# Performance work log

Measured on AMD Instinct MI355X. Metric: run time of the kernel, lower is better.

Reference implementation:

```python
import jax, jax.numpy as jnp
import numpy as np

S, N, V, E, H, L = 40, 256, 32000, 1024, 1024, 2


def _gru_step(x, h, wih, whh, bih, bhh):
    # PyTorch GRU cell, gate order [r, z, n]
    gi = x @ wih.T + bih          # (N, 3H)
    gh = h @ whh.T + bhh          # (N, 3H)
    ir, iz, inn = jnp.split(gi, 3, axis=-1)
    hr, hz, hn = jnp.split(gh, 3, axis=-1)
    r = jax.nn.sigmoid(ir + hr)
    z = jax.nn.sigmoid(iz + hz)
    n = jnp.tanh(inn + r * hn)
    return (1.0 - z) * n + z * h


def setup_inputs() -> dict:
    key = jax.random.key(0)
    ks = jax.random.split(key, 16)
    nrm = lambda k, shp: (jax.random.normal(k, shp, jnp.float32) * 0.05)
    return {
        "tokens": jax.random.randint(ks[0], (S, N), 0, V),
        "hidden": jnp.zeros((L, N, H), jnp.float32),
        "emb": nrm(ks[1], (V, E)),
        "enc_wih": nrm(ks[2], (L, 3 * H, E)),
        "enc_whh": nrm(ks[3], (L, 3 * H, H)),
        "enc_bih": nrm(ks[4], (L, 3 * H)),
        "enc_bhh": nrm(ks[5], (L, 3 * H)),
        "dec_wih": nrm(ks[6], (L, 3 * H, H)),
        "dec_whh": nrm(ks[7], (L, 3 * H, H)),
        "dec_bih": nrm(ks[8], (L, 3 * H)),
        "dec_bhh": nrm(ks[9], (L, 3 * H)),
        "attn_w": nrm(ks[10], (S, E + L * H)),
        "attn_b": nrm(ks[11], (S,)),
        "comb_w": nrm(ks[12], (H, 2 * H)),
        "comb_b": nrm(ks[13], (H,)),
    }


def reference(tokens, hidden, emb, enc_wih, enc_whh, enc_bih, enc_bhh,
              dec_wih, dec_whh, dec_bih, dec_bhh,
              attn_w, attn_b, comb_w, comb_b):
    x = emb[tokens]                      # (S, N, E) embedded input

    # ---- encoder: 2-layer GRU over the full sequence ----
    seq = x
    h_finals = []
    for l in range(L):
        wih, whh, bih, bhh = enc_wih[l], enc_whh[l], enc_bih[l], enc_bhh[l]
        def step(h, xt, wih=wih, whh=whh, bih=bih, bhh=bhh):
            h2 = _gru_step(xt, h, wih, whh, bih, bhh)
            return h2, h2
        hT, seq = jax.lax.scan(step, hidden[l], seq)
        h_finals.append(hT)
    h_n = jnp.stack(h_finals)            # (L, N, H)
    enc_out = jnp.swapaxes(seq, 0, 1)    # (N, S, H)

    # ---- attention decoder: scan over timesteps, carry decoder hidden ----
    def dec_step(h, emb_t):
        # h: (L, N, H), emb_t: (N, E)
        h_flat = jnp.swapaxes(h, 0, 1).reshape(N, L * H)
        logits = jnp.concatenate([emb_t, h_flat], axis=-1) @ attn_w.T + attn_b
        aw = jax.nn.softmax(logits, axis=-1)                   # (N, S)
        applied = jnp.einsum('ns,nsh->nh', aw, enc_out)        # (N, H)
        xcur = jax.nn.relu(
            jnp.concatenate([emb_t, applied], axis=-1) @ comb_w.T + comb_b)
        hs = []
        for l in range(L):
            hl = _gru_step(xcur, h[l], dec_wih[l], dec_whh[l],
                           dec_bih[l], dec_bhh[l])
            hs.append(hl)
            xcur = hl
        return jnp.stack(hs), xcur

    hT, outs = jax.lax.scan(dec_step, h_n, x)   # outs: (S, N, H)
    return outs, hT
```

## Files before the change

### kernel.cpp

```cpp
#include <hip/hip_runtime.h>
#include <hip/hip_bf16.h>

#define S_LEN 40
#define NB    256
#define EDIM  1024
#define HDIM  1024
#define NBLK  256
#define NTHR  768

typedef _Float16 f16;
typedef __attribute__((ext_vector_type(8))) _Float16 f16x8;
typedef __attribute__((ext_vector_type(4))) _Float16 f16x4;
typedef __attribute__((ext_vector_type(4))) float f32x4;

__device__ __forceinline__ float sigm(float x) {
    x = fminf(fmaxf(x, -30.f), 30.f);
    return 1.f / (1.f + __expf(-x));
}
__device__ __forceinline__ float tanh_fast(float x) {
    x = fminf(fmaxf(x, -15.f), 15.f);
    float e = __expf(2.f * x);
    return (e - 1.f) / (e + 1.f);
}

__device__ __forceinline__ void sysst_f16(f16* p, f16 v) {
    union { f16 f; unsigned short s; } u; u.f = v;
    unsigned int b = u.s;
    asm volatile("global_store_short %0, %1, off sc0 sc1" :: "v"(p), "v"(b) : "memory");
}

__device__ __forceinline__ void gbar1(unsigned* cnt, unsigned* gen) {
    asm volatile("s_waitcnt vmcnt(0)" ::: "memory");
    __syncthreads();
    if (threadIdx.x == 0) {
        unsigned g = __hip_atomic_load(gen, __ATOMIC_RELAXED, __HIP_MEMORY_SCOPE_AGENT);
        unsigned a = __hip_atomic_fetch_add(cnt, 1u, __ATOMIC_RELEASE, __HIP_MEMORY_SCOPE_AGENT);
        if (a == NBLK - 1) {
            __hip_atomic_store(cnt, 0u, __ATOMIC_RELAXED, __HIP_MEMORY_SCOPE_AGENT);
            __hip_atomic_fetch_add(gen, 1u, __ATOMIC_RELEASE, __HIP_MEMORY_SCOPE_AGENT);
        } else {
            while (__hip_atomic_load(gen, __ATOMIC_RELAXED, __HIP_MEMORY_SCOPE_AGENT) == g)
                __builtin_amdgcn_s_sleep(1);
        }
    }
    __syncthreads();
}

__device__ __forceinline__ void g2bar(unsigned* sync, unsigned xcd,
                                      unsigned M, unsigned NX) {
    asm volatile("s_waitcnt vmcnt(0)" ::: "memory");
    __syncthreads();
    if (threadIdx.x == 0) {
        unsigned* ggen = sync;
        unsigned* gcnt = sync + 1;
        unsigned* xa = sync + 16 + xcd * 16;
        unsigned g = __hip_atomic_load(ggen, __ATOMIC_RELAXED, __HIP_MEMORY_SCOPE_AGENT);
        unsigned a = __hip_atomic_fetch_add(xa, 1u, __ATOMIC_RELEASE, __HIP_MEMORY_SCOPE_AGENT);
        if (a == M - 1) {
            __hip_atomic_store(xa, 0u, __ATOMIC_RELAXED, __HIP_MEMORY_SCOPE_AGENT);
            unsigned b = __hip_atomic_fetch_add(gcnt, 1u, __ATOMIC_RELEASE, __HIP_MEMORY_SCOPE_AGENT);
            if (b == NX - 1) {
                __hip_atomic_store(gcnt, 0u, __ATOMIC_RELAXED, __HIP_MEMORY_SCOPE_AGENT);
                __hip_atomic_fetch_add(ggen, 1u, __ATOMIC_RELEASE, __HIP_MEMORY_SCOPE_AGENT);
            } else {
                while (__hip_atomic_load(ggen, __ATOMIC_RELAXED, __HIP_MEMORY_SCOPE_AGENT) == g)
                    __builtin_amdgcn_s_sleep(1);
            }
        } else {
            while (__hip_atomic_load(ggen, __ATOMIC_RELAXED, __HIP_MEMORY_SCOPE_AGENT) == g)
                __builtin_amdgcn_s_sleep(1);
        }
    }
    __syncthreads();
}

__global__ void k_init_sync(unsigned* s) {
    for (int k = threadIdx.x; k < 1024; k += 256) s[k] = 0;
}

__device__ __forceinline__ void probe_mn(int lane, int* mrow, int* ncol) {
    f16x8 pa, pb;
#pragma unroll
    for (int e = 0; e < 8; e++) {
        pa[e] = (f16)(float)(lane & 15);
        pb[e] = (f16)0.03125f;
    }
    f32x4 pacc = {0, 0, 0, 0};
    pacc = __builtin_amdgcn_mfma_f32_16x16x32_f16(pa, pb, pacc, 0, 0, 0);
#pragma unroll
    for (int r = 0; r < 4; r++) {
        int m = (int)(pacc[r] + 0.5f);
        int cg = ((lane >> 4) << 2) + r;
        mrow[r] = m;
        ncol[r] = (m == cg) ? (lane & 15) : cg;
    }
}

__global__ __launch_bounds__(256) void k_cvt4(const float* __restrict__ src,
                                              f16* __restrict__ dst, int n4) {
    int i = blockIdx.x * 256 + threadIdx.x;
    if (i < n4) {
        f32x4 v = ((const f32x4*)src)[i];
        f16x4 o = {(f16)v.x, (f16)v.y, (f16)v.z, (f16)v.w};
        ((f16x4*)dst)[i] = o;
    }
}
__global__ __launch_bounds__(256) void k_embed_cvt(const int* __restrict__ tok,
                                                   const float* __restrict__ emb,
                                                   f16* __restrict__ xe) {
    int b = blockIdx.x;
    int t = threadIdx.x;
    int token = tok[b];
    f32x4 v = ((const f32x4*)(emb + (size_t)token * EDIM))[t];
    f16x4 o = {(f16)v.x, (f16)v.y, (f16)v.z, (f16)v.w};
    ((f16x4*)(xe + (size_t)b * EDIM))[t] = o;
}

__device__ void gru_phase(
    char* lds, int cb, int rb, int tid, const int* mr, const int* nc,
    const f16* __restrict__ xsrc, const f16* __restrict__ hsrc,
    const f16* __restrict__ wih, const f16* __restrict__ whh,
    const float* __restrict__ bih, const float* __restrict__ bhh,
    f16* ho16, float* of_step, float* of_fin) {

    {
        constexpr int TOT = 8192;
        constexpr int IT = (TOT + NTHR - 1) / NTHR;
        f16x8 val[IT];
#pragma unroll
        for (int i = 0; i < IT; i++) {
            int c = tid + i * NTHR;
            if (c < TOT) {
                int isH = c >> 12;
                int cl = c & 4095;
                int row = cl >> 7, cc = cl & 127;
                const f16* src = (isH ? hsrc : xsrc) +
                                 (size_t)(rb + row) * 1024 + cc * 8;
                val[i] = *(const f16x8*)src;
            }
        }
#pragma unroll
        for (int i = 0; i < IT; i++) {
            int c = tid + i * NTHR;
            if (c < TOT) {
                int isH = c >> 12;
                int cl = c & 4095;
                int row = cl >> 7, cc = cl & 127;
                *(f16x8*)(lds + isH * 65536 + row * 2048 +
                          ((cc ^ (row & 7)) << 4)) = val[i];
            }
        }
    }
    __syncthreads();

    const int w = tid >> 6, lane = tid & 63;
    const int pair = w >> 1, kh = w & 1;
    const int gate = (pair >= 3) ? pair - 3 : pair;
    const int r0 = lane & 15, kk0 = (lane >> 4) * 8;
    const f16* B = ((pair < 3) ? wih : whh) + ((size_t)gate * HDIM + cb) * 1024;
    const f16* B0 = B + (size_t)r0 * 1024 + kk0 + kh * 512;
    const f16* B1 = B + (size_t)(r0 + 16) * 1024 + kk0 + kh * 512;
    const int abase = (pair < 3) ? 0 : 65536;
    const int swz = r0 & 7;
    const char* a0p = lds + abase + r0 * 2048;
    const char* a1p = lds + abase + (r0 + 16) * 2048;

    f32x4 acc00 = {0,0,0,0}, acc01 = {0,0,0,0}, acc10 = {0,0,0,0}, acc11 = {0,0,0,0};
#pragma unroll 4
    for (int k = 0; k < 512; k += 32) {
        int g = (kh * 512 + kk0 + k) >> 3;
        int off = (g ^ swz) << 4;
        f16x8 a0 = *(const f16x8*)(a0p + off);
        f16x8 a1 = *(const f16x8*)(a1p + off);
        f16x8 b0 = *(const f16x8*)(B0 + k);
        f16x8 b1 = *(const f16x8*)(B1 + k);
        acc00 = __builtin_amdgcn_mfma_f32_16x16x32_f16(a0, b0, acc00, 0, 0, 0);
        acc01 = __builtin_amdgcn_mfma_f32_16x16x32_f16(a0, b1, acc01, 0, 0, 0);
        acc10 = __builtin_amdgcn_mfma_f32_16x16x32_f16(a1, b0, acc10, 0, 0, 0);
        acc11 = __builtin_amdgcn_mfma_f32_16x16x32_f16(a1, b1, acc11, 0, 0, 0);
    }
    __syncthreads();

    float* red = (float*)lds;
    float* rw = red + w * 1024;
#pragma unroll
    for (int r = 0; r < 4; r++) {
        rw[mr[r] * 32 + nc[r]]             = acc00[r];
        rw[mr[r] * 32 + nc[r] + 16]        = acc01[r];
        rw[(mr[r] + 16) * 32 + nc[r]]      = acc10[r];
        rw[(mr[r] + 16) * 32 + nc[r] + 16] = acc11[r];
    }
    __syncthreads();

#pragma unroll
    for (int it = 0; it < 2; it++) {
        int i = tid + it * NTHR;
        if (i < 1024) {
            int rr = i >> 5, ccn = i & 31;
            int col = cb + ccn;
            int row = rb + rr;
            float gir = red[i]         + red[1024 + i];
            float giz = red[2048 + i]  + red[3072 + i];
            float gin = red[4096 + i]  + red[5120 + i];
            float ghr = red[6144 + i]  + red[7168 + i];
            float ghz = red[8192 + i]  + red[9216 + i];
            float ghn = red[10240 + i] + red[11264 + i];
            float r = sigm(gir + bih[col] + ghr + bhh[col]);
            float z = sigm(giz + bih[HDIM + col] + ghz + bhh[HDIM + col]);
            float n = tanh_fast(gin + bih[2 * HDIM + col] +
                                r * (ghn + bhh[2 * HDIM + col]));
            int gidx = col >> 3, within = col & 7;
            float hp = (float)*(const f16*)(lds + 65536 + rr * 2048 +
                                            ((gidx ^ (rr & 7)) << 4) + within * 2);
            float hn2 = (1.f - z) * n + z * hp;
            size_t idx = (size_t)row * HDIM + col;
            sysst_f16(ho16 + idx, (f16)hn2);
            if (of_step) of_step[idx] = hn2;
            if (of_fin)  of_fin[idx] = hn2;
        }
    }
}

__device__ void attn_phase(
    char* lds, int bid, int tid,
    const f16* __restrict__ xe_t, const f16* __restrict__ h0,
    const f16* __restrict__ h1,
    const f16* __restrict__ attn_w, const float* __restrict__ attn_b,
    const f16* __restrict__ enc16, f16* __restrict__ appl) {
    float* logit = (float*)(lds + 131072);
    float* awls  = logit + 64;
    const int n = bid;
    const int w = tid >> 6, lane = tid & 63;
    const size_t nrow = (size_t)n * 1024;

    {
        constexpr int TOT = 5504;
        constexpr int IT = (TOT + NTHR - 1) / NTHR;
        f16x8 val[IT];
#pragma unroll
        for (int i = 0; i < IT; i++) {
            int c = tid + i * NTHR;
            if (c < TOT) {
                if (c < 5120) {
                    int s = c >> 7, cc = c & 127;
                    val[i] = __builtin_nontemporal_load(
                        (const f16x8*)(enc16 + ((size_t)s * NB + n) * 1024 + cc * 8));
                } else {
                    int r = c - 5120;
                    const f16* src = (r < 128) ? (xe_t + nrow + r * 8)
                                   : (r < 256) ? (h0 + nrow + (r - 128) * 8)
                                               : (h1 + nrow + (r - 256) * 8);
                    val[i] = *(const f16x8*)src;
                }
            }
        }
#pragma unroll
        for (int i = 0; i < IT; i++) {
            int c = tid + i * NTHR;
            if (c < TOT) {
                if (c < 5120) *(f16x8*)(lds + c * 16) = val[i];
                else          *(f16x8*)(lds + 81920 + (c - 5120) * 16) = val[i];
            }
        }
    }
    __syncthreads();

    if (w < 10) {
#pragma unroll
        for (int si = 0; si < 4; si++) {
            int s = w * 4 + si;
            const f16* wrow = attn_w + (size_t)s * 3072;
            float acc = 0.f;
#pragma unroll
            for (int jj = 0; jj < 6; jj++) {
                int j = lane + jj * 64;
                f16x8 a = *(const f16x8*)(lds + 81920 + j * 16);
                f16x8 b = __builtin_nontemporal_load((const f16x8*)(wrow + j * 8));
#pragma unroll
                for (int e = 0; e < 8; e++)
                    acc = fmaf((float)a[e], (float)b[e], acc);
            }
            for (int o = 32; o; o >>= 1) acc += __shfl_down(acc, o);
            if (lane == 0) logit[s] = acc + attn_b[s];
        }
    }
    __syncthreads();

    if (w == 0) {
        float v = (lane < S_LEN) ? logit[lane] : -1e30f;
        float m = v;
        for (int o = 32; o; o >>= 1) m = fmaxf(m, __shfl_xor(m, o));
        float e = (lane < S_LEN) ? __expf(v - m) : 0.f;
        float sum = e;
        for (int o = 32; o; o >>= 1) sum += __shfl_xor(sum, o);
        if (lane < S_LEN) awls[lane] = e / sum;
    }
    __syncthreads();

    for (int col = tid; col < 1024; col += NTHR) {
        float acc = 0.f;
#pragma unroll
        for (int s = 0; s < S_LEN; s++)
            acc = fmaf(awls[s], (float)*(const f16*)(lds + s * 2048 + col * 2), acc);
        sysst_f16(appl + nrow + col, (f16)acc);
    }
}

__device__ void comb_phase(
    char* lds, int cb, int rb, int tid, const int* mr, const int* nc,
    const f16* __restrict__ xe_t, const f16* __restrict__ appl,
    const f16* __restrict__ Bw, const float* __restrict__ bias,
    f16* __restrict__ Cout) {

    {
        constexpr int TOT = 8192;
        constexpr int IT = (TOT + NTHR - 1) / NTHR;
        f16x8 val[IT];
#pragma unroll
        for (int i = 0; i < IT; i++) {
            int c = tid + i * NTHR;
            if (c < TOT) {
                int row = c >> 8, cc = c & 255;
                const f16* src = (cc < 128)
                    ? (xe_t + (size_t)(rb + row) * 1024 + cc * 8)
                    : (appl + (size_t)(rb + row) * 1024 + (cc - 128) * 8);
                val[i] = *(const f16x8*)src;
            }
        }
#pragma unroll
        for (int i = 0; i < IT; i++) {
            int c = tid + i * NTHR;
            if (c < TOT) {
                int row = c >> 8, cc = c & 255;
                *(f16x8*)(lds + row * 4096 + ((cc ^ (row & 7)) << 4)) = val[i];
            }
        }
    }
    __syncthreads();

    const int w = tid >> 6, lane = tid & 63;
    const int r0 = lane & 15, kk0 = (lane >> 4) * 8;
    const int c0 = (w * 64) / 12, c1 = ((w + 1) * 64) / 12;
    const f16* B0 = Bw + (size_t)(cb + r0) * 2048 + kk0;
    const f16* B1 = Bw + (size_t)(cb + r0 + 16) * 2048 + kk0;
    const int swz = r0 & 7;
    const char* a0p = lds + r0 * 4096;
    const char* a1p = lds + (r0 + 16) * 4096;

    f32x4 acc00 = {0,0,0,0}, acc01 = {0,0,0,0}, acc10 = {0,0,0,0}, acc11 = {0,0,0,0};
    for (int c = c0; c < c1; c++) {
        int g = (c * 32 + kk0) >> 3;
        int off = (g ^ swz) << 4;
        f16x8 a0 = *(const f16x8*)(a0p + off);
        f16x8 a1 = *(const f16x8*)(a1p + off);
        f16x8 b0 = *(const f16x8*)(B0 + c * 32);
        f16x8 b1 = *(const f16x8*)(B1 + c * 32);
        acc00 = __builtin_amdgcn_mfma_f32_16x16x32_f16(a0, b0, acc00, 0, 0, 0);
        acc01 = __builtin_amdgcn_mfma_f32_16x16x32_f16(a0, b1, acc01, 0, 0, 0);
        acc10 = __builtin_amdgcn_mfma_f32_16x16x32_f16(a1, b0, acc10, 0, 0, 0);
        acc11 = __builtin_amdgcn_mfma_f32_16x16x32_f16(a1, b1, acc11, 0, 0, 0);
    }
    __syncthreads();

    float* red = (float*)lds;
    float* rw = red + w * 1024;
#pragma unroll
    for (int r = 0; r < 4; r++) {
        rw[mr[r] * 32 + nc[r]]             = acc00[r];
        rw[mr[r] * 32 + nc[r] + 16]        = acc01[r];
        rw[(mr[r] + 16) * 32 + nc[r]]      = acc10[r];
        rw[(mr[r] + 16) * 32 + nc[r] + 16] = acc11[r];
    }
    __syncthreads();

#pragma unroll
    for (int it = 0; it < 2; it++) {
        int i = tid + it * NTHR;
        if (i < 1024) {
            float s = 0.f;
#pragma unroll
            for (int p = 0; p < 12; p++) s += red[p * 1024 + i];
            int rr = i >> 5, ccn = i & 31;
            s += bias[cb + ccn];
            s = fmaxf(s, 0.f);
            sysst_f16(Cout + (size_t)(rb + rr) * 1024 + cb + ccn, (f16)s);
        }
    }
}

__global__ __launch_bounds__(NTHR, 3) void k_mega(
    const f16* __restrict__ xe,
    f16* H0, f16* H1,
    const f16* __restrict__ w_eih, const f16* __restrict__ w_ehh,
    const float* __restrict__ enc_bih, const float* __restrict__ enc_bhh,
    const f16* __restrict__ w_dih, const f16* __restrict__ w_dhh,
    const float* __restrict__ dec_bih, const float* __restrict__ dec_bhh,
    const f16* __restrict__ w_attn, const float* __restrict__ attn_b,
    const f16* __restrict__ w_comb, const float* __restrict__ comb_b,
    f16* XC, f16* AP,
    float* out, unsigned* sync) {
    __shared__ char smem[131584];
    __shared__ unsigned s_meta[8];
    char* lds = smem;
    const int bid = blockIdx.x;
    const int tid = threadIdx.x;
    const int lane = tid & 63;
    const size_t NH = (size_t)NB * HDIM;

    int mr[4], nc[4];
    probe_mn(lane, mr, nc);

    if (tid == 0) {
        unsigned x;
        asm volatile("s_getreg_b32 %0, hwreg(20, 0, 32)" : "=s"(x));
        x &= 7;
        unsigned r = __hip_atomic_fetch_add(sync + 256 + x, 1u,
                                            __ATOMIC_RELAXED, __HIP_MEMORY_SCOPE_AGENT);
        s_meta[0] = x; s_meta[1] = r;
    }
    __syncthreads();
    gbar1(sync + 512, sync + 513);
    if (tid == 0) {
        unsigned M = __hip_atomic_load(sync + 256 + s_meta[0],
                                       __ATOMIC_RELAXED, __HIP_MEMORY_SCOPE_AGENT);
        unsigned nx = 0;
        bool uniform = true;
        for (int i = 0; i < 8; i++) {
            unsigned ci = __hip_atomic_load(sync + 256 + i, __ATOMIC_RELAXED,
                                            __HIP_MEMORY_SCOPE_AGENT);
            nx += (ci > 0) ? 1u : 0u;
            if (ci != 32) uniform = false;
        }
        s_meta[2] = M; s_meta[3] = nx;
        if (uniform) {
            s_meta[4] = (s_meta[0] * 4 + (s_meta[1] & 3)) * 32;
            s_meta[5] = (s_meta[1] >> 2) * 32;
        } else {
            s_meta[4] = (((unsigned)bid & 7) * 4 + (((unsigned)bid >> 3) & 3)) * 32;
            s_meta[5] = ((unsigned)bid >> 5) * 32;
        }
    }
    __syncthreads();
    const unsigned xcd = s_meta[0], M = s_meta[2], NX = s_meta[3];
    const int cb = (int)s_meta[4], rb = (int)s_meta[5];

    for (int t = 0; t < S_LEN; t++) {
        gru_phase(lds, cb, rb, tid, mr, nc,
                  xe + (size_t)t * NB * EDIM, H0 + (size_t)t * NH,
                  w_eih, w_ehh, enc_bih, enc_bhh,
                  H0 + (size_t)(t + 1) * NH, (float*)nullptr, (float*)nullptr);
        g2bar(sync, xcd, M, NX);
    }
    for (int t = 0; t < S_LEN; t++) {
        gru_phase(lds, cb, rb, tid, mr, nc,
                  H0 + (size_t)(t + 1) * NH, H1 + (size_t)t * NH,
                  w_eih + (size_t)3 * HDIM * EDIM, w_ehh + (size_t)3 * HDIM * HDIM,
                  enc_bih + 3 * HDIM, enc_bhh + 3 * HDIM,
                  H1 + (size_t)(t + 1) * NH, (float*)nullptr, (float*)nullptr);
        g2bar(sync, xcd, M, NX);
    }

    for (int t = 0; t < S_LEN; t++) {
        int g = S_LEN + t;
        attn_phase(lds, bid, tid,
                   xe + (size_t)t * NB * EDIM,
                   H0 + (size_t)g * NH, H1 + (size_t)g * NH,
                   w_attn, attn_b, H1 + NH, AP + (size_t)t * NH);
        g2bar(sync, xcd, M, NX);
        comb_phase(lds, cb, rb, tid, mr, nc,
                   xe + (size_t)t * NB * EDIM, AP + (size_t)t * NH,
                   w_comb, comb_b, XC + (size_t)t * NH);
        g2bar(sync, xcd, M, NX);
        gru_phase(lds, cb, rb, tid, mr, nc,
                  XC + (size_t)t * NH, H0 + (size_t)g * NH,
                  w_dih, w_dhh, dec_bih, dec_bhh,
                  H0 + (size_t)(g + 1) * NH, (float*)nullptr,
                  (t == S_LEN - 1) ? (out + (size_t)S_LEN * NH) : (float*)nullptr);
        g2bar(sync, xcd, M, NX);
        gru_phase(lds, cb, rb, tid, mr, nc,
                  H0 + (size_t)(g + 1) * NH, H1 + (size_t)g * NH,
                  w_dih + (size_t)3 * HDIM * HDIM, w_dhh + (size_t)3 * HDIM * HDIM,
                  dec_bih + 3 * HDIM, dec_bhh + 3 * HDIM,
                  H1 + (size_t)(g + 1) * NH, out + (size_t)t * NH,
                  (t == S_LEN - 1) ? (out + (size_t)(S_LEN + 1) * NH) : (float*)nullptr);
        g2bar(sync, xcd, M, NX);
    }
}

extern "C" void kernel_launch(void* const* d_in, const int* in_sizes, int n_in,
                              void* d_out, int out_size, void* d_ws, size_t ws_size,
                              hipStream_t stream) {
    const int*   tokens   = (const int*)d_in[0];
    const float* hidden   = (const float*)d_in[1];
    const float* emb      = (const float*)d_in[2];
    const float* enc_wih  = (const float*)d_in[3];
    const float* enc_whh  = (const float*)d_in[4];
    const float* enc_bih  = (const float*)d_in[5];
    const float* enc_bhh  = (const float*)d_in[6];
    const float* dec_wih  = (const float*)d_in[7];
    const float* dec_whh  = (const float*)d_in[8];
    const float* dec_bih  = (const float*)d_in[9];
    const float* dec_bhh  = (const float*)d_in[10];
    const float* attn_w   = (const float*)d_in[11];
    const float* attn_b   = (const float*)d_in[12];
    const float* comb_w   = (const float*)d_in[13];
    const float* comb_b   = (const float*)d_in[14];
    float* out = (float*)d_out;

    const size_t NH = (size_t)NB * HDIM;
    const size_t WSZ = (size_t)2 * 3 * HDIM * EDIM;

    f16* wp = (f16*)d_ws;
    f16 *w_eih = wp;  wp += WSZ;
    f16 *w_ehh = wp;  wp += WSZ;
    f16 *w_dih = wp;  wp += WSZ;
    f16 *w_dhh = wp;  wp += WSZ;
    f16 *w_comb = wp; wp += (size_t)HDIM * 2048;
    f16 *w_attn = wp; wp += (size_t)S_LEN * 3072;
    f16 *xe = wp;     wp += (size_t)S_LEN * NB * EDIM;
    f16 *H0 = wp;     wp += (size_t)(2 * S_LEN + 1) * NH;
    f16 *H1 = wp;     wp += (size_t)(2 * S_LEN + 1) * NH;
    f16 *XC = wp;     wp += (size_t)S_LEN * NH;
    f16 *AP = wp;     wp += (size_t)S_LEN * NH;
    unsigned* syncp = (unsigned*)((((uintptr_t)wp) + 255) & ~(uintptr_t)255);

    k_init_sync<<<1, 256, 0, stream>>>(syncp);

    k_cvt4<<<(int)(WSZ / 4 / 256), 256, 0, stream>>>(enc_wih, w_eih, (int)(WSZ / 4));
    k_cvt4<<<(int)(WSZ / 4 / 256), 256, 0, stream>>>(enc_whh, w_ehh, (int)(WSZ / 4));
    k_cvt4<<<(int)(WSZ / 4 / 256), 256, 0, stream>>>(dec_wih, w_dih, (int)(WSZ / 4));
    k_cvt4<<<(int)(WSZ / 4 / 256), 256, 0, stream>>>(dec_whh, w_dhh, (int)(WSZ / 4));
    k_cvt4<<<(int)(HDIM * 2048 / 4 / 256), 256, 0, stream>>>(comb_w, w_comb,
                                                             HDIM * 2048 / 4);
    k_cvt4<<<(S_LEN * 3072 / 4 + 255) / 256, 256, 0, stream>>>(attn_w, w_attn,
                                                               S_LEN * 3072 / 4);
    k_embed_cvt<<<S_LEN * NB, 256, 0, stream>>>(tokens, emb, xe);
    k_cvt4<<<(int)(NH / 4 / 256), 256, 0, stream>>>(hidden, H0, (int)(NH / 4));
    k_cvt4<<<(int)(NH / 4 / 256), 256, 0, stream>>>(hidden + NH, H1, (int)(NH / 4));

    k_mega<<<NBLK, NTHR, 0, stream>>>(
        xe, H0, H1,
        w_eih, w_ehh, enc_bih, enc_bhh,
        w_dih, w_dhh, dec_bih, dec_bhh,
        w_attn, attn_b, w_comb, comb_b,
        XC, AP, out, syncp);
}
```

Measured before the change: 5.838 ms.

## Replace grid-wide barrier with per-batch-row-group barriers and remap attention rows

```diff
diff --git a/kernel.cpp b/kernel.cpp
--- a/kernel.cpp
+++ b/kernel.cpp
@@ -46,28 +46,19 @@
     __syncthreads();
 }
 
-__device__ __forceinline__ void g2bar(unsigned* sync, unsigned xcd,
-                                      unsigned M, unsigned NX) {
+__device__ __forceinline__ void grbar(unsigned* sync, unsigned grp) {
     asm volatile("s_waitcnt vmcnt(0)" ::: "memory");
     __syncthreads();
     if (threadIdx.x == 0) {
-        unsigned* ggen = sync;
-        unsigned* gcnt = sync + 1;
-        unsigned* xa = sync + 16 + xcd * 16;
-        unsigned g = __hip_atomic_load(ggen, __ATOMIC_RELAXED, __HIP_MEMORY_SCOPE_AGENT);
-        unsigned a = __hip_atomic_fetch_add(xa, 1u, __ATOMIC_RELEASE, __HIP_MEMORY_SCOPE_AGENT);
-        if (a == M - 1) {
-            __hip_atomic_store(xa, 0u, __ATOMIC_RELAXED, __HIP_MEMORY_SCOPE_AGENT);
-            unsigned b = __hip_atomic_fetch_add(gcnt, 1u, __ATOMIC_RELEASE, __HIP_MEMORY_SCOPE_AGENT);
-            if (b == NX - 1) {
-                __hip_atomic_store(gcnt, 0u, __ATOMIC_RELAXED, __HIP_MEMORY_SCOPE_AGENT);
-                __hip_atomic_fetch_add(ggen, 1u, __ATOMIC_RELEASE, __HIP_MEMORY_SCOPE_AGENT);
-            } else {
-                while (__hip_atomic_load(ggen, __ATOMIC_RELAXED, __HIP_MEMORY_SCOPE_AGENT) == g)
-                    __builtin_amdgcn_s_sleep(1);
-            }
+        unsigned* cnt = sync + 32 + grp * 16;
+        unsigned* gen = sync + 33 + grp * 16;
+        unsigned g = __hip_atomic_load(gen, __ATOMIC_RELAXED, __HIP_MEMORY_SCOPE_AGENT);
+        unsigned a = __hip_atomic_fetch_add(cnt, 1u, __ATOMIC_RELEASE, __HIP_MEMORY_SCOPE_AGENT);
+        if (a == 31u) {
+            __hip_atomic_store(cnt, 0u, __ATOMIC_RELAXED, __HIP_MEMORY_SCOPE_AGENT);
+            __hip_atomic_fetch_add(gen, 1u, __ATOMIC_RELEASE, __HIP_MEMORY_SCOPE_AGENT);
         } else {
-            while (__hip_atomic_load(ggen, __ATOMIC_RELAXED, __HIP_MEMORY_SCOPE_AGENT) == g)
+            while (__hip_atomic_load(gen, __ATOMIC_RELAXED, __HIP_MEMORY_SCOPE_AGENT) == g)
                 __builtin_amdgcn_s_sleep(1);
         }
     }
@@ -222,14 +213,13 @@
 }
 
 __device__ void attn_phase(
-    char* lds, int bid, int tid,
+    char* lds, int n, int tid,
     const f16* __restrict__ xe_t, const f16* __restrict__ h0,
     const f16* __restrict__ h1,
     const f16* __restrict__ attn_w, const float* __restrict__ attn_b,
     const f16* __restrict__ enc16, f16* __restrict__ appl) {
     float* logit = (float*)(lds + 131072);
     float* awls  = logit + 64;
-    const int n = bid;
     const int w = tid >> 6, lane = tid & 63;
     const size_t nrow = (size_t)n * 1024;
 
@@ -243,8 +233,7 @@
             if (c < TOT) {
                 if (c < 5120) {
                     int s = c >> 7, cc = c & 127;
-                    val[i] = __builtin_nontemporal_load(
-                        (const f16x8*)(enc16 + ((size_t)s * NB + n) * 1024 + cc * 8));
+                    val[i] = *(const f16x8*)(enc16 + ((size_t)s * NB + n) * 1024 + cc * 8);
                 } else {
                     int r = c - 5120;
                     const f16* src = (r < 128) ? (xe_t + nrow + r * 8)
@@ -275,7 +264,7 @@
             for (int jj = 0; jj < 6; jj++) {
                 int j = lane + jj * 64;
                 f16x8 a = *(const f16x8*)(lds + 81920 + j * 16);
-                f16x8 b = __builtin_nontemporal_load((const f16x8*)(wrow + j * 8));
+                f16x8 b = *(const f16x8*)(wrow + j * 8);
 #pragma unroll
                 for (int e = 0; e < 8; e++)
                     acc = fmaf((float)a[e], (float)b[e], acc);
@@ -421,17 +410,12 @@
     __syncthreads();
     gbar1(sync + 512, sync + 513);
     if (tid == 0) {
-        unsigned M = __hip_atomic_load(sync + 256 + s_meta[0],
-                                       __ATOMIC_RELAXED, __HIP_MEMORY_SCOPE_AGENT);
-        unsigned nx = 0;
         bool uniform = true;
         for (int i = 0; i < 8; i++) {
             unsigned ci = __hip_atomic_load(sync + 256 + i, __ATOMIC_RELAXED,
                                             __HIP_MEMORY_SCOPE_AGENT);
-            nx += (ci > 0) ? 1u : 0u;
             if (ci != 32) uniform = false;
         }
-        s_meta[2] = M; s_meta[3] = nx;
         if (uniform) {
             s_meta[4] = (s_meta[0] * 4 + (s_meta[1] & 3)) * 32;
             s_meta[5] = (s_meta[1] >> 2) * 32;
@@ -441,15 +425,16 @@
         }
     }
     __syncthreads();
-    const unsigned xcd = s_meta[0], M = s_meta[2], NX = s_meta[3];
     const int cb = (int)s_meta[4], rb = (int)s_meta[5];
+    const unsigned grp = (unsigned)rb >> 5;
+    const int arow = rb + (cb >> 5);
 
     for (int t = 0; t < S_LEN; t++) {
         gru_phase(lds, cb, rb, tid, mr, nc,
                   xe + (size_t)t * NB * EDIM, H0 + (size_t)t * NH,
                   w_eih, w_ehh, enc_bih, enc_bhh,
                   H0 + (size_t)(t + 1) * NH, (float*)nullptr, (float*)nullptr);
-        g2bar(sync, xcd, M, NX);
+        grbar(sync, grp);
     }
     for (int t = 0; t < S_LEN; t++) {
         gru_phase(lds, cb, rb, tid, mr, nc,
@@ -457,33 +442,33 @@
                   w_eih + (size_t)3 * HDIM * EDIM, w_ehh + (size_t)3 * HDIM * HDIM,
                   enc_bih + 3 * HDIM, enc_bhh + 3 * HDIM,
                   H1 + (size_t)(t + 1) * NH, (float*)nullptr, (float*)nullptr);
-        g2bar(sync, xcd, M, NX);
+        grbar(sync, grp);
     }
 
     for (int t = 0; t < S_LEN; t++) {
         int g = S_LEN + t;
-        attn_phase(lds, bid, tid,
+        attn_phase(lds, arow, tid,
                    xe + (size_t)t * NB * EDIM,
                    H0 + (size_t)g * NH, H1 + (size_t)g * NH,
                    w_attn, attn_b, H1 + NH, AP + (size_t)t * NH);
-        g2bar(sync, xcd, M, NX);
+        grbar(sync, grp);
         comb_phase(lds, cb, rb, tid, mr, nc,
                    xe + (size_t)t * NB * EDIM, AP + (size_t)t * NH,
                    w_comb, comb_b, XC + (size_t)t * NH);
-        g2bar(sync, xcd, M, NX);
+        grbar(sync, grp);
         gru_phase(lds, cb, rb, tid, mr, nc,
                   XC + (size_t)t * NH, H0 + (size_t)g * NH,
                   w_dih, w_dhh, dec_bih, dec_bhh,
                   H0 + (size_t)(g + 1) * NH, (float*)nullptr,
                   (t == S_LEN - 1) ? (out + (size_t)S_LEN * NH) : (float*)nullptr);
-        g2bar(sync, xcd, M, NX);
+        grbar(sync, grp);
         gru_phase(lds, cb, rb, tid, mr, nc,
                   H0 + (size_t)(g + 1) * NH, H1 + (size_t)g * NH,
                   w_dih + (size_t)3 * HDIM * HDIM, w_dhh + (size_t)3 * HDIM * HDIM,
                   dec_bih + 3 * HDIM, dec_bhh + 3 * HDIM,
                   H1 + (size_t)(g + 1) * NH, out + (size_t)t * NH,
                   (t == S_LEN - 1) ? (out + (size_t)(S_LEN + 1) * NH) : (float*)nullptr);
-        g2bar(sync, xcd, M, NX);
+        grbar(sync, grp);
     }
 }
 
```

Result: no change. 5.909 ms (+1.2%).
